# Performance work log

Measured on AMD Instinct MI355X. Metric: run time of the kernel, lower is better.

The kernel has to match this reference:

```python
import jax, jax.numpy as jnp
import numpy as np

D_MODEL = 1024
N_LAYERS = 4
EXPAND = 2
D_CONV = 4
D_STATE = 16
INTER = EXPAND * D_MODEL          # 2048
DT_RANK = (D_MODEL + 15) // 16    # 64, HF: math.ceil(d_model/16)
B_SZ = 4
SEQ = 1024
EPS = 1e-5


def setup_inputs() -> dict:
    key = jax.random.key(0)
    ks = jax.random.split(key, 8)
    nrm = lambda k, s: (0.02 * jax.random.normal(k, s)).astype(jnp.float32)
    return {
        "x": jax.random.normal(ks[0], (B_SZ, SEQ, D_MODEL), dtype=jnp.float32),
        "in_w": nrm(ks[1], (N_LAYERS, 2 * INTER, D_MODEL)),           # in_proj (no bias)
        "conv_w": nrm(ks[2], (N_LAYERS, INTER, D_CONV)),              # depthwise conv weight
        "conv_b": jnp.zeros((N_LAYERS, INTER), jnp.float32),           # conv bias
        "x_w": nrm(ks[3], (N_LAYERS, DT_RANK + 2 * D_STATE, INTER)),  # x_proj (no bias)
        "dt_w": nrm(ks[4], (N_LAYERS, INTER, DT_RANK)),               # dt_proj weight
        "dt_b": jax.random.uniform(ks[5], (N_LAYERS, INTER), minval=-4.0, maxval=-2.0).astype(jnp.float32),
        "A_log": jnp.tile(jnp.log(jnp.arange(1, D_STATE + 1, dtype=jnp.float32)), (N_LAYERS, INTER, 1)),
        "D": jnp.ones((N_LAYERS, INTER), jnp.float32),
        "out_w": nrm(ks[6], (N_LAYERS, D_MODEL, INTER)),              # out_proj (no bias)
        "norm_w": jnp.ones((N_LAYERS, D_MODEL), jnp.float32),          # per-block RMSNorm
        "norm_f_w": jnp.ones((D_MODEL,), jnp.float32),                 # final RMSNorm
    }


def _rmsnorm(x, w):
    return x * jax.lax.rsqrt(jnp.mean(x * x, axis=-1, keepdims=True) + EPS) * w


def _mixer(x, in_w, conv_w, conv_b, x_w, dt_w, dt_b, A_log, Dp, out_w):
    # x: [B, L, d_model]
    Bb = x.shape[0]
    proj = x @ in_w.T                              # [B, L, 2I]
    hs, gate = jnp.split(proj, 2, axis=-1)          # each [B, L, I]
    # causal depthwise conv over time
    hc = hs.transpose(0, 2, 1)                      # [B, I, L]
    hc = jnp.pad(hc, ((0, 0), (0, 0), (D_CONV - 1, 0)))
    hc = jax.lax.conv_general_dilated(
        hc, conv_w[:, None, :], (1,), 'VALID',
        dimension_numbers=('NCH', 'OIH', 'NCH'), feature_group_count=INTER)
    hc = hc + conv_b[None, :, None]
    u = jax.nn.silu(hc).transpose(0, 2, 1)          # [B, L, I]
    ssm = u @ x_w.T                                 # [B, L, dt_rank + 2N]
    dt, Bm, Cm = jnp.split(ssm, [DT_RANK, DT_RANK + D_STATE], axis=-1)
    dt = jax.nn.softplus(dt @ dt_w.T + dt_b)        # [B, L, I]
    A = -jnp.exp(A_log)                             # [I, N]

    def step(state, xs):
        dt_t, B_t, C_t, u_t = xs                    # [B,I], [B,N], [B,N], [B,I]
        dA = jnp.exp(dt_t[:, :, None] * A[None])    # [B, I, N]
        state = dA * state + (dt_t * u_t)[:, :, None] * B_t[:, None, :]
        y = jnp.einsum('bin,bn->bi', state, C_t)
        return state, y

    init = jnp.zeros((Bb, INTER, D_STATE), x.dtype)
    xs = (dt.transpose(1, 0, 2), Bm.transpose(1, 0, 2),
          Cm.transpose(1, 0, 2), u.transpose(1, 0, 2))
    _, ys = jax.lax.scan(step, init, xs)            # ys: [L, B, I]
    y = ys.transpose(1, 0, 2) + u * Dp              # skip term D * u
    y = y * jax.nn.silu(gate)
    return y @ out_w.T                              # [B, L, d_model]


def reference(x, in_w, conv_w, conv_b, x_w, dt_w, dt_b, A_log, D, out_w, norm_w, norm_f_w):
    h = x
    for l in range(N_LAYERS):
        h = h + _mixer(_rmsnorm(h, norm_w[l]), in_w[l], conv_w[l], conv_b[l],
                       x_w[l], dt_w[l], dt_b[l], A_log[l], D[l], out_w[l])
    return _rmsnorm(h, norm_f_w)
```

## Files before the change

### kernel.cpp

```cpp
#include <hip/hip_runtime.h>
#include <hip/hip_bf16.h>
#include <math.h>

#define D_MODEL 1024
#define N_LAYERS 4
#define INTER 2048
#define D_CONV 4
#define D_STATE 16
#define DT_RANK 64
#define B_SZ 4
#define SEQ 1024
#define TOK (B_SZ*SEQ)
#define XROWS 128
#define EPSV 1e-5f
#define GCH 64
#define TC (SEQ/GCH)
#define KSPL 8
#define OSPL 2

typedef unsigned short u16;
typedef unsigned int u32;
typedef __attribute__((ext_vector_type(8))) short bf16x8;
typedef __attribute__((ext_vector_type(4))) short s16x4;
typedef __attribute__((ext_vector_type(4))) float f32x4;

__device__ __forceinline__ u16 f2b(float f) {
    union { float f; unsigned u; } v; v.f = f;
    unsigned r = v.u + 0x7fffu + ((v.u >> 16) & 1u);
    return (u16)(r >> 16);
}
__device__ __forceinline__ float b2f(u16 h) {
    union { unsigned u; float f; } v; v.u = ((unsigned)h) << 16;
    return v.f;
}
__device__ __forceinline__ float silu(float x) {
    return x / (1.f + __expf(-x));
}
__device__ __forceinline__ void gload16(const void* g, void* l) {
    __builtin_amdgcn_global_load_lds(
        (const __attribute__((address_space(1))) void*)g,
        (__attribute__((address_space(3))) void*)l, 16, 0, 0);
}

__global__ __launch_bounds__(512, 2)
void gemm256_k(const u16* __restrict__ A, const u16* __restrict__ B,
               u16* __restrict__ C, int K, int ldc)
{
    __shared__ u16 lds[2][2][256 * 64];
    const int tid  = threadIdx.x;
    const int lane = tid & 63;
    const int wid  = tid >> 6;
    const int wr   = wid >> 2;
    const int wc   = wid & 3;
    const int row0 = blockIdx.y * 256;
    const int col0 = blockIdx.x * 256;
    const int r16   = lane & 15;
    const int khalf = lane >> 4;

    auto stage = [&](int buf, int k0) {
#pragma unroll
        for (int l = 0; l < 8; ++l) {
            int op = l >> 2;
            int c  = tid + (l & 3) * 512;
            int r  = c >> 3;
            int ds = c & 7;
            int sc = (ds ^ (r & 7)) * 8;
            const u16* src = op ? &B[(size_t)(col0 + r) * K + k0 + sc]
                                : &A[(size_t)(row0 + r) * K + k0 + sc];
            gload16(src, &lds[buf][op][c * 8]);
        }
    };
    auto rdA = [&](int buf, int mrow, int ks) -> bf16x8 {
        int row  = wr * 128 + mrow + r16;
        int phys = ((ks << 2) | khalf) ^ (row & 7);
        return *(const bf16x8*)&lds[buf][0][row * 64 + phys * 8];
    };
    auto rdB = [&](int buf, int nrow, int ks) -> bf16x8 {
        int row  = wc * 64 + nrow + r16;
        int phys = ((ks << 2) | khalf) ^ (row & 7);
        return *(const bf16x8*)&lds[buf][1][row * 64 + phys * 8];
    };

    f32x4 acc[8][4];
#pragma unroll
    for (int m = 0; m < 8; ++m)
#pragma unroll
        for (int n = 0; n < 4; ++n)
            acc[m][n] = (f32x4)0.f;

    bf16x8 af[4][2], bf2[2][2];

#define PHASE_MFMA(MH, NH, VMDRAIN) do {                                      \
    asm volatile("s_waitcnt lgkmcnt(0)" ::: "memory");                        \
    __builtin_amdgcn_sched_barrier(0);                                        \
    __builtin_amdgcn_s_setprio(1);                                            \
    _Pragma("unroll")                                                         \
    for (int ks = 0; ks < 2; ++ks)                                            \
        _Pragma("unroll")                                                     \
        for (int m = 0; m < 4; ++m)                                           \
            _Pragma("unroll")                                                 \
            for (int n = 0; n < 2; ++n)                                       \
                acc[(MH)*4+m][(NH)*2+n] =                                     \
                    __builtin_amdgcn_mfma_f32_16x16x32_bf16(                  \
                        af[m][ks], bf2[n][ks], acc[(MH)*4+m][(NH)*2+n],0,0,0);\
    __builtin_amdgcn_s_setprio(0);                                            \
    if (VMDRAIN) { asm volatile("s_waitcnt vmcnt(0)" ::: "memory"); }         \
    __builtin_amdgcn_s_barrier();                                             \
} while (0)

    const int nt = K >> 6;
    stage(0, 0);
    asm volatile("s_waitcnt vmcnt(0)" ::: "memory");
    __builtin_amdgcn_s_barrier();

    for (int j = 0; j < nt; ++j) {
        const int buf = j & 1;
        if (j + 1 < nt) stage(buf ^ 1, (j + 1) << 6);
#pragma unroll
        for (int m = 0; m < 4; ++m) {
            af[m][0] = rdA(buf, m * 16, 0); af[m][1] = rdA(buf, m * 16, 1);
        }
#pragma unroll
        for (int n = 0; n < 2; ++n) {
            bf2[n][0] = rdB(buf, n * 16, 0); bf2[n][1] = rdB(buf, n * 16, 1);
        }
        __builtin_amdgcn_s_barrier();
        PHASE_MFMA(0, 0, 0);
#pragma unroll
        for (int n = 0; n < 2; ++n) {
            bf2[n][0] = rdB(buf, 32 + n * 16, 0); bf2[n][1] = rdB(buf, 32 + n * 16, 1);
        }
        __builtin_amdgcn_s_barrier();
        PHASE_MFMA(0, 1, 0);
#pragma unroll
        for (int m = 0; m < 4; ++m) {
            af[m][0] = rdA(buf, 64 + m * 16, 0); af[m][1] = rdA(buf, 64 + m * 16, 1);
        }
        __builtin_amdgcn_s_barrier();
        PHASE_MFMA(1, 1, 0);
#pragma unroll
        for (int n = 0; n < 2; ++n) {
            bf2[n][0] = rdB(buf, n * 16, 0); bf2[n][1] = rdB(buf, n * 16, 1);
        }
        __builtin_amdgcn_s_barrier();
        PHASE_MFMA(1, 0, 1);
    }
#undef PHASE_MFMA

    const int orow = row0 + wr * 128;
    const int ocol = col0 + wc * 64;
#pragma unroll
    for (int am = 0; am < 8; ++am)
#pragma unroll
        for (int an = 0; an < 4; ++an)
#pragma unroll
            for (int r = 0; r < 4; ++r) {
                int rr = orow + am * 16 + khalf * 4 + r;
                int cc = ocol + an * 16 + r16;
                C[(size_t)rr * ldc + cc] = f2b(acc[am][an][r]);
            }
}

template<int EPI, int NPX = 1>
__global__ __launch_bounds__(256)
void gemm_bt(const u16* __restrict__ A, const u16* __restrict__ B,
             void* __restrict__ C, const float* __restrict__ aux,
             int K, int lda, int ldc, size_t pstride)
{
    __shared__ u16 As[3][128 * 32];
    __shared__ u16 Bs[3][128 * 32];
    const int tid  = threadIdx.x;
    const int lane = tid & 63;
    const int w    = tid >> 6;
    const int wr   = w >> 1, wc = w & 1;
    const int row0 = blockIdx.y * 128;
    int col0 = blockIdx.x * 128;
    if (EPI == 4) {
        int part = blockIdx.x / NPX;
        col0 = (blockIdx.x % NPX) * 128;
        A += (size_t)part * K;
        B += (size_t)part * K;
        C = (void*)((float*)C + (size_t)part * pstride);
    }
    const int r16   = lane & 15;
    const int khalf = lane >> 4;
    const int kslot = khalf ^ ((r16 >> 1) & 3);

    auto stage = [&](int buf, int k0) {
#pragma unroll
        for (int c = 0; c < 2; ++c) {
            int chunk = tid + c * 256;
            int r  = chunk >> 2;
            int j  = chunk & 3;
            int k8 = (j ^ ((r >> 1) & 3)) * 8;
            gload16(&A[(size_t)(row0 + r) * lda + k0 + k8], &As[buf][chunk * 8]);
            gload16(&B[(size_t)(col0 + r) * lda + k0 + k8], &Bs[buf][chunk * 8]);
        }
    };

    f32x4 acc[4][4];
#pragma unroll
    for (int m = 0; m < 4; ++m)
#pragma unroll
        for (int n = 0; n < 4; ++n)
            acc[m][n] = (f32x4)0.f;

    const int nt = K >> 5;
    stage(0, 0);
    if (nt > 1) stage(1, 32);

    int cur = 0, sb = 2;
    for (int t = 0; t < nt; ++t) {
        if (t + 2 < nt) {
            stage(sb, (t + 2) << 5);
            asm volatile("s_waitcnt vmcnt(8)" ::: "memory");
        } else if (t + 1 < nt) {
            asm volatile("s_waitcnt vmcnt(4)" ::: "memory");
        } else {
            asm volatile("s_waitcnt vmcnt(0)" ::: "memory");
        }
        __builtin_amdgcn_s_barrier();

        bf16x8 af[4], bfr[4];
#pragma unroll
        for (int m = 0; m < 4; ++m)
            af[m]  = *(const bf16x8*)&As[cur][(wr * 64 + m * 16 + r16) * 32 + kslot * 8];
#pragma unroll
        for (int n = 0; n < 4; ++n)
            bfr[n] = *(const bf16x8*)&Bs[cur][(wc * 64 + n * 16 + r16) * 32 + kslot * 8];
#pragma unroll
        for (int m = 0; m < 4; ++m)
#pragma unroll
            for (int n = 0; n < 4; ++n)
                acc[m][n] = __builtin_amdgcn_mfma_f32_16x16x32_bf16(
                    af[m], bfr[n], acc[m][n], 0, 0, 0);

        __builtin_amdgcn_sched_barrier(0);
        asm volatile("s_waitcnt lgkmcnt(0)" ::: "memory");
        __builtin_amdgcn_s_barrier();
        cur = (cur == 2) ? 0 : cur + 1;
        sb  = (sb  == 2) ? 0 : sb  + 1;
    }

    const int orow = row0 + wr * 64;
    const int ocol = col0 + wc * 64;
#pragma unroll
    for (int m = 0; m < 4; ++m)
#pragma unroll
        for (int n = 0; n < 4; ++n) {
#pragma unroll
            for (int r = 0; r < 4; ++r) {
                int rr = orow + m * 16 + khalf * 4 + r;
                int cc = ocol + n * 16 + r16;
                float v = acc[m][n][r];
                size_t o = (size_t)rr * ldc + cc;
                if (EPI == 0 || EPI == 4) {
                    ((float*)C)[o] = v;
                } else if (EPI == 2) {
                    float x = v + aux[cc];
                    float sp = (x > 20.f) ? x : log1pf(__expf(x));
                    ((u16*)C)[o] = f2b(sp);
                }
            }
        }
}

__global__ __launch_bounds__(256)
void xred_k(const float* __restrict__ part, float* __restrict__ ssm,
            u16* __restrict__ dtr)
{
    int idx = blockIdx.x * 256 + threadIdx.x;
    int row = idx >> 5;
    int col = (idx & 31) * 4;
    size_t o = (size_t)row * XROWS + col;
    const size_t stride = (size_t)TOK * XROWS;
    f32x4 v = *(const f32x4*)&part[o];
#pragma unroll
    for (int p = 1; p < KSPL; ++p)
        v += *(const f32x4*)&part[o + p * stride];
    *(f32x4*)&ssm[o] = v;
    if (col < DT_RANK) {
        s16x4 d;
#pragma unroll
        for (int j = 0; j < 4; ++j) d[j] = (short)f2b(v[j]);
        *(s16x4*)&dtr[(size_t)row * DT_RANK + col] = d;
    }
}

template<int OUTBF>
__global__ __launch_bounds__(256)
void rmsnorm_k(const float* __restrict__ in, const float* __restrict__ w,
               void* __restrict__ out)
{
    __shared__ float red[4];
    const int row = blockIdx.x;
    const int tid = threadIdx.x;
    const float* r = in + (size_t)row * D_MODEL;
    f32x4 v = *(const f32x4*)&r[tid * 4];
    float ss = v[0]*v[0] + v[1]*v[1] + v[2]*v[2] + v[3]*v[3];
#pragma unroll
    for (int m = 32; m >= 1; m >>= 1) ss += __shfl_xor(ss, m, 64);
    if ((tid & 63) == 0) red[tid >> 6] = ss;
    __syncthreads();
    if (tid == 0) {
        float s = red[0] + red[1] + red[2] + red[3];
        red[0] = rsqrtf(s / (float)D_MODEL + EPSV);
    }
    __syncthreads();
    float sc = red[0];
    if (OUTBF) {
        u16* o = (u16*)out + (size_t)row * D_MODEL + tid * 4;
#pragma unroll
        for (int j = 0; j < 4; ++j) o[j] = f2b(v[j] * sc * w[tid * 4 + j]);
    } else {
        float* o = (float*)out + (size_t)row * D_MODEL + tid * 4;
#pragma unroll
        for (int j = 0; j < 4; ++j) o[j] = v[j] * sc * w[tid * 4 + j];
    }
}

template<int OUTBF, int WRITEH>
__global__ __launch_bounds__(256)
void rmsnorm_res_k(const float* __restrict__ hin, const float* __restrict__ p,
                   const float* __restrict__ w, float* __restrict__ hout,
                   void* __restrict__ out)
{
    __shared__ float red[4];
    const int row = blockIdx.x;
    const int tid = threadIdx.x;
    const size_t o4 = (size_t)row * D_MODEL + tid * 4;
    f32x4 v  = *(const f32x4*)&hin[o4];
    f32x4 p0 = *(const f32x4*)&p[o4];
    f32x4 p1 = *(const f32x4*)&p[(size_t)TOK * D_MODEL + o4];
    v += p0 + p1;
    if (WRITEH) *(f32x4*)&hout[o4] = v;
    float ss = v[0]*v[0] + v[1]*v[1] + v[2]*v[2] + v[3]*v[3];
#pragma unroll
    for (int m = 32; m >= 1; m >>= 1) ss += __shfl_xor(ss, m, 64);
    if ((tid & 63) == 0) red[tid >> 6] = ss;
    __syncthreads();
    if (tid == 0) {
        float s = red[0] + red[1] + red[2] + red[3];
        red[0] = rsqrtf(s / (float)D_MODEL + EPSV);
    }
    __syncthreads();
    float sc = red[0];
    if (OUTBF) {
        u16* o = (u16*)out + o4;
#pragma unroll
        for (int j = 0; j < 4; ++j) o[j] = f2b(v[j] * sc * w[tid * 4 + j]);
    } else {
        float* o = (float*)out + o4;
#pragma unroll
        for (int j = 0; j < 4; ++j) o[j] = v[j] * sc * w[tid * 4 + j];
    }
}

__global__ __launch_bounds__(256)
void conv_silu_k(const u16* __restrict__ projbf, const float* __restrict__ w,
                 const float* __restrict__ bias, u16* __restrict__ ubf)
{
    const int row = blockIdx.x;
    const int t   = row & (SEQ - 1);
    const int i0  = threadIdx.x * 8;
    float acc[8];
    {
        f32x4 b0 = *(const f32x4*)&bias[i0];
        f32x4 b1 = *(const f32x4*)&bias[i0 + 4];
#pragma unroll
        for (int j = 0; j < 4; ++j) { acc[j] = b0[j]; acc[j + 4] = b1[j]; }
    }
    f32x4 wv[8];
#pragma unroll
    for (int j = 0; j < 8; ++j)
        wv[j] = *(const f32x4*)&w[(i0 + j) * 4];
#pragma unroll
    for (int k = 0; k < 4; ++k) {
        int tt = t - 3 + k;
        if (tt >= 0) {
            bf16x8 hv = *(const bf16x8*)&projbf[(size_t)(row - 3 + k) * 4096 + i0];
#pragma unroll
            for (int j = 0; j < 8; ++j)
                acc[j] += b2f((u16)hv[j]) * wv[j][k];
        }
    }
    bf16x8 o;
#pragma unroll
    for (int j = 0; j < 8; ++j)
        o[j] = (short)f2b(silu(acc[j]));
    *(bf16x8*)&ubf[(size_t)row * INTER + i0] = o;
}

__global__ __launch_bounds__(256)
void achk_k(const float* __restrict__ Alog, int* __restrict__ flags)
{
    int idx = blockIdx.x * 256 + threadIdx.x;
    if (idx >= N_LAYERS * INTER * D_STATE) return;
    int l = idx / (INTER * D_STATE);
    int n = idx & (D_STATE - 1);
    float ref = logf((float)(n + 1));
    if (fabsf(Alog[idx] - ref) > 1e-4f) atomicAnd(&flags[l], 0);
}

#define POWCH(W, p) \
    float p##2=(W)*(W), p##3=p##2*(W), p##4=p##2*p##2, p##5=p##4*(W),        \
          p##6=p##4*p##2, p##7=p##4*p##3, p##8=p##4*p##4, p##9=p##8*(W),     \
          p##10=p##8*p##2, p##11=p##8*p##3, p##12=p##8*p##4, p##13=p##8*p##5,\
          p##14=p##8*p##6, p##15=p##8*p##7, p##16=p##8*p##8;

#define SUPD(S, B, du, w1) \
    S[0]=w1*S[0]+du*B[0][0];   S[1]=w1##2*S[1]+du*B[0][1];                   \
    S[2]=w1##3*S[2]+du*B[0][2];  S[3]=w1##4*S[3]+du*B[0][3];                 \
    S[4]=w1##5*S[4]+du*B[1][0];  S[5]=w1##6*S[5]+du*B[1][1];                 \
    S[6]=w1##7*S[6]+du*B[1][2];  S[7]=w1##8*S[7]+du*B[1][3];                 \
    S[8]=w1##9*S[8]+du*B[2][0];  S[9]=w1##10*S[9]+du*B[2][1];                \
    S[10]=w1##11*S[10]+du*B[2][2]; S[11]=w1##12*S[11]+du*B[2][3];            \
    S[12]=w1##13*S[12]+du*B[3][0]; S[13]=w1##14*S[13]+du*B[3][1];            \
    S[14]=w1##15*S[14]+du*B[3][2]; S[15]=w1##16*S[15]+du*B[3][3];

#define YDOT(S, Cv) \
    (S[0]*Cv[0][0]+S[1]*Cv[0][1]+S[2]*Cv[0][2]+S[3]*Cv[0][3]                 \
    +S[4]*Cv[1][0]+S[5]*Cv[1][1]+S[6]*Cv[1][2]+S[7]*Cv[1][3]                 \
    +S[8]*Cv[2][0]+S[9]*Cv[2][1]+S[10]*Cv[2][2]+S[11]*Cv[2][3]               \
    +S[12]*Cv[3][0]+S[13]*Cv[3][1]+S[14]*Cv[3][2]+S[15]*Cv[3][3])

__global__ __launch_bounds__(256)
void scan1_k(const u16* __restrict__ dtbf, const u16* __restrict__ ubf,
             const float* __restrict__ ssm, const float* __restrict__ Alog,
             const int* __restrict__ flag,
             float* __restrict__ cst, float* __restrict__ dts)
{
    __shared__ float Bsh[TC][D_STATE];
    const int tid = threadIdx.x;
    const int i2  = blockIdx.x * 256 + tid;
    const int c0  = i2 * 2;
    const int g   = blockIdx.y;
    const int b   = blockIdx.z;
    const int t0  = g * TC;
    {
        int t = tid >> 4, n = tid & 15;
        Bsh[t][n] = ssm[(size_t)(b * SEQ + t0 + t) * XROWS + DT_RANK + n];
    }
    __syncthreads();

    float s0[D_STATE], s1[D_STATE];
#pragma unroll
    for (int n = 0; n < D_STATE; ++n) { s0[n] = 0.f; s1[n] = 0.f; }
    float ds0 = 0.f, ds1 = 0.f;

    const u32* dtp = (const u32*)dtbf + ((size_t)(b * SEQ + t0) * INTER >> 1) + i2;
    const u32* up  = (const u32*)ubf  + ((size_t)(b * SEQ + t0) * INTER >> 1) + i2;

    if (flag[0]) {
#pragma unroll
        for (int t = 0; t < TC; ++t) {
            u32 dp = dtp[(size_t)t * (INTER / 2)];
            u32 uq = up[(size_t)t * (INTER / 2)];
            float dta = b2f((u16)dp), dtb = b2f((u16)(dp >> 16));
            float ua  = b2f((u16)uq), ub  = b2f((u16)(uq >> 16));
            float dua = dta * ua, dub = dtb * ub;
            ds0 += dta; ds1 += dtb;
            float wa = __expf(-dta), wb = __expf(-dtb);
            POWCH(wa, wa) POWCH(wb, wb)
            f32x4 Bq[4];
#pragma unroll
            for (int q = 0; q < 4; ++q) Bq[q] = *(const f32x4*)&Bsh[t][q * 4];
            SUPD(s0, Bq, dua, wa)
            SUPD(s1, Bq, dub, wb)
        }
    } else {
        float a0[D_STATE], a1[D_STATE];
#pragma unroll
        for (int n = 0; n < D_STATE; ++n) {
            a0[n] = -__expf(Alog[(size_t)c0 * D_STATE + n]);
            a1[n] = -__expf(Alog[(size_t)(c0 + 1) * D_STATE + n]);
        }
        for (int t = 0; t < TC; ++t) {
            u32 dp = dtp[(size_t)t * (INTER / 2)];
            u32 uq = up[(size_t)t * (INTER / 2)];
            float dta = b2f((u16)dp), dtb = b2f((u16)(dp >> 16));
            float ua  = b2f((u16)uq), ub  = b2f((u16)(uq >> 16));
            float dua = dta * ua, dub = dtb * ub;
            ds0 += dta; ds1 += dtb;
#pragma unroll
            for (int n = 0; n < D_STATE; ++n) {
                float Bn = Bsh[t][n];
                s0[n] = __expf(dta * a0[n]) * s0[n] + dua * Bn;
                s1[n] = __expf(dtb * a1[n]) * s1[n] + dub * Bn;
            }
        }
    }
    size_t o = ((size_t)(b * GCH + g) * INTER + c0) * D_STATE;
#pragma unroll
    for (int n = 0; n < D_STATE; n += 4) {
        f32x4 v0 = { s0[n], s0[n+1], s0[n+2], s0[n+3] };
        f32x4 v1 = { s1[n], s1[n+1], s1[n+2], s1[n+3] };
        *(f32x4*)&cst[o + n] = v0;
        *(f32x4*)&cst[o + D_STATE + n] = v1;
    }
    size_t od = (size_t)(b * GCH + g) * INTER + c0;
    dts[od] = ds0; dts[od + 1] = ds1;
}

__global__ __launch_bounds__(256)
void scan2_k(float* __restrict__ cst, const float* __restrict__ dts,
             const float* __restrict__ Alog)
{
    int idx = blockIdx.x * 256 + threadIdx.x;
    int sub = idx & 3;
    int i   = (idx >> 2) & (INTER - 1);
    int b   = idx >> 13;
    int n0  = sub * 4;
    float a[4];
#pragma unroll
    for (int n = 0; n < 4; ++n)
        a[n] = -__expf(Alog[(size_t)i * D_STATE + n0 + n]);
    f32x4 s = (f32x4)0.f;
    for (int g = 0; g < GCH; ++g) {
        size_t o = ((size_t)(b * GCH + g) * INTER + i) * D_STATE + n0;
        f32x4 tmp = *(const f32x4*)&cst[o];
        *(f32x4*)&cst[o] = s;
        float d = dts[(size_t)(b * GCH + g) * INTER + i];
#pragma unroll
        for (int n = 0; n < 4; ++n)
            s[n] = __expf(a[n] * d) * s[n] + tmp[n];
    }
}

__global__ __launch_bounds__(256)
void scan3_k(const u16* __restrict__ dtbf, const u16* __restrict__ ubf,
             const float* __restrict__ ssm, const u16* __restrict__ projbf,
             const float* __restrict__ Alog, const float* __restrict__ Dp,
             const int* __restrict__ flag,
             const float* __restrict__ sst, u16* __restrict__ ybf)
{
    __shared__ float Bsh[TC][D_STATE];
    __shared__ float Csh[TC][D_STATE];
    const int tid = threadIdx.x;
    const int i2  = blockIdx.x * 256 + tid;
    const int c0  = i2 * 2;
    const int g   = blockIdx.y;
    const int b   = blockIdx.z;
    const int t0  = g * TC;
    {
        int t = tid >> 4, n = tid & 15;
        size_t row = (size_t)(b * SEQ + t0 + t) * XROWS;
        Bsh[t][n] = ssm[row + DT_RANK + n];
        Csh[t][n] = ssm[row + DT_RANK + D_STATE + n];
    }
    __syncthreads();

    const float Da = Dp[c0], Db = Dp[c0 + 1];
    float s0[D_STATE], s1[D_STATE];
    size_t so = ((size_t)(b * GCH + g) * INTER + c0) * D_STATE;
#pragma unroll
    for (int n = 0; n < D_STATE; n += 4) {
        f32x4 v0 = *(const f32x4*)&sst[so + n];
        f32x4 v1 = *(const f32x4*)&sst[so + D_STATE + n];
        s0[n] = v0[0]; s0[n+1] = v0[1]; s0[n+2] = v0[2]; s0[n+3] = v0[3];
        s1[n] = v1[0]; s1[n+1] = v1[1]; s1[n+2] = v1[2]; s1[n+3] = v1[3];
    }

    const u32* dtp = (const u32*)dtbf + ((size_t)(b * SEQ + t0) * INTER >> 1) + i2;
    const u32* up  = (const u32*)ubf  + ((size_t)(b * SEQ + t0) * INTER >> 1) + i2;
    const u32* gp  = (const u32*)projbf + (((size_t)(b * SEQ + t0) * 4096 + INTER) >> 1) + i2;
    u32*       yp  = (u32*)ybf + ((size_t)(b * SEQ + t0) * INTER >> 1) + i2;

    if (flag[0]) {
#pragma unroll
        for (int t = 0; t < TC; ++t) {
            u32 dp = dtp[(size_t)t * (INTER / 2)];
            u32 uq = up[(size_t)t * (INTER / 2)];
            u32 gq = gp[(size_t)t * (4096 / 2)];
            float dta = b2f((u16)dp), dtb = b2f((u16)(dp >> 16));
            float ua  = b2f((u16)uq), ub  = b2f((u16)(uq >> 16));
            float ga  = b2f((u16)gq), gb  = b2f((u16)(gq >> 16));
            float dua = dta * ua, dub = dtb * ub;
            float wa = __expf(-dta), wb = __expf(-dtb);
            POWCH(wa, wa) POWCH(wb, wb)
            f32x4 Bq[4], Cq[4];
#pragma unroll
            for (int q = 0; q < 4; ++q) {
                Bq[q] = *(const f32x4*)&Bsh[t][q * 4];
                Cq[q] = *(const f32x4*)&Csh[t][q * 4];
            }
            SUPD(s0, Bq, dua, wa)
            SUPD(s1, Bq, dub, wb)
            float y0 = YDOT(s0, Cq);
            float y1 = YDOT(s1, Cq);
            y0 = (y0 + Da * ua) * silu(ga);
            y1 = (y1 + Db * ub) * silu(gb);
            yp[(size_t)t * (INTER / 2)] = (u32)f2b(y0) | ((u32)f2b(y1) << 16);
        }
    } else {
        float a0[D_STATE], a1[D_STATE];
#pragma unroll
        for (int n = 0; n < D_STATE; ++n) {
            a0[n] = -__expf(Alog[(size_t)c0 * D_STATE + n]);
            a1[n] = -__expf(Alog[(size_t)(c0 + 1) * D_STATE + n]);
        }
        for (int t = 0; t < TC; ++t) {
            u32 dp = dtp[(size_t)t * (INTER / 2)];
            u32 uq = up[(size_t)t * (INTER / 2)];
            u32 gq = gp[(size_t)t * (4096 / 2)];
            float dta = b2f((u16)dp), dtb = b2f((u16)(dp >> 16));
            float ua  = b2f((u16)uq), ub  = b2f((u16)(uq >> 16));
            float ga  = b2f((u16)gq), gb  = b2f((u16)(gq >> 16));
            float dua = dta * ua, dub = dtb * ub;
            float y0 = 0.f, y1 = 0.f;
#pragma unroll
            for (int n = 0; n < D_STATE; ++n) {
                float Bn = Bsh[t][n], Cn = Csh[t][n];
                s0[n] = __expf(dta * a0[n]) * s0[n] + dua * Bn;
                s1[n] = __expf(dtb * a1[n]) * s1[n] + dub * Bn;
                y0 += s0[n] * Cn; y1 += s1[n] * Cn;
            }
            y0 = (y0 + Da * ua) * silu(ga);
            y1 = (y1 + Db * ub) * silu(gb);
            yp[(size_t)t * (INTER / 2)] = (u32)f2b(y0) | ((u32)f2b(y1) << 16);
        }
    }
}

__global__ __launch_bounds__(256)
void cvt_f2b_k(const float* __restrict__ in, u16* __restrict__ out, int n)
{
    int idx = (blockIdx.x * 256 + threadIdx.x) * 4;
    if (idx >= n) return;
    f32x4 v = *(const f32x4*)&in[idx];
    s16x4 d;
#pragma unroll
    for (int j = 0; j < 4; ++j) d[j] = (short)f2b(v[j]);
    *(s16x4*)&out[idx] = d;
}

__global__ __launch_bounds__(256)
void pad_xw_k(const float* __restrict__ xw, u16* __restrict__ out)
{
    int idx = (blockIdx.x * 256 + threadIdx.x) * 4;
    if (idx >= N_LAYERS * XROWS * INTER) return;
    int l = idx / (XROWS * INTER);
    int r = (idx >> 11) & (XROWS - 1);
    int c = idx & (INTER - 1);
    s16x4 d;
    if (r < 96) {
        f32x4 v = *(const f32x4*)&xw[((size_t)l * 96 + r) * INTER + c];
#pragma unroll
        for (int j = 0; j < 4; ++j) d[j] = (short)f2b(v[j]);
    } else {
        d = (s16x4)0;
    }
    *(s16x4*)&out[idx] = d;
}

extern "C" void kernel_launch(void* const* d_in, const int* in_sizes, int n_in,
                              void* d_out, int out_size, void* d_ws, size_t ws_size,
                              hipStream_t stream)
{
    const float* x      = (const float*)d_in[0];
    const float* in_w   = (const float*)d_in[1];
    const float* conv_w = (const float*)d_in[2];
    const float* conv_b = (const float*)d_in[3];
    const float* x_w    = (const float*)d_in[4];
    const float* dt_w   = (const float*)d_in[5];
    const float* dt_b   = (const float*)d_in[6];
    const float* A_log  = (const float*)d_in[7];
    const float* Dp     = (const float*)d_in[8];
    const float* out_w  = (const float*)d_in[9];
    const float* norm_w = (const float*)d_in[10];
    const float* norm_f = (const float*)d_in[11];

    char* ws = (char*)d_ws;
    size_t off = 0;
    auto alloc = [&](size_t bytes) { char* p = ws + off; off += (bytes + 255) & ~(size_t)255; return p; };

    u16*   inw_bf  = (u16*)  alloc((size_t)N_LAYERS * 4096 * 1024 * 2);
    u16*   xw_bf   = (u16*)  alloc((size_t)N_LAYERS * XROWS * INTER * 2);
    u16*   dtw_bf  = (u16*)  alloc((size_t)N_LAYERS * INTER * DT_RANK * 2);
    u16*   outw_bf = (u16*)  alloc((size_t)N_LAYERS * D_MODEL * INTER * 2);
    float* h       = (float*)alloc((size_t)TOK * D_MODEL * 4);
    u16*   xn_bf   = (u16*)  alloc((size_t)TOK * D_MODEL * 2);
    u16*   proj_bf = (u16*)  alloc((size_t)TOK * 4096 * 2);
    u16*   u_bf    = (u16*)  alloc((size_t)TOK * INTER * 2);
    float* ssm     = (float*)alloc((size_t)TOK * XROWS * 4);
    float* parts   = (float*)alloc((size_t)OSPL * TOK * D_MODEL * 4);
    u16*   dtr_bf  = (u16*)  alloc((size_t)TOK * DT_RANK * 2);
    u16*   dt_bf   = (u16*)  alloc((size_t)TOK * INTER * 2);
    u16*   y_bf    = (u16*)  alloc((size_t)TOK * INTER * 2);
    float* cst     = (float*)alloc((size_t)B_SZ * GCH * INTER * D_STATE * 4);
    float* dts     = (float*)alloc((size_t)B_SZ * GCH * INTER * 4);
    int*   aflags  = (int*)  alloc(N_LAYERS * sizeof(int));
    (void)ws_size; (void)n_in; (void)in_sizes; (void)out_size;

    {
        int n = N_LAYERS * 4096 * 1024;
        cvt_f2b_k<<<n / 1024, 256, 0, stream>>>(in_w, inw_bf, n);
        int np = N_LAYERS * XROWS * INTER;
        pad_xw_k<<<np / 1024, 256, 0, stream>>>(x_w, xw_bf);
        int nd = N_LAYERS * INTER * DT_RANK;
        cvt_f2b_k<<<nd / 1024, 256, 0, stream>>>(dt_w, dtw_bf, nd);
        int no = N_LAYERS * D_MODEL * INTER;
        cvt_f2b_k<<<no / 1024, 256, 0, stream>>>(out_w, outw_bf, no);
        hipMemsetAsync(aflags, 0xFF, N_LAYERS * sizeof(int), stream);
        int na = N_LAYERS * INTER * D_STATE;
        achk_k<<<(na + 255) / 256, 256, 0, stream>>>(A_log, aflags);
    }

    for (int l = 0; l < N_LAYERS; ++l) {
        if (l == 0)
            rmsnorm_k<1><<<TOK, 256, 0, stream>>>(x, norm_w, xn_bf);
        else
            rmsnorm_res_k<1, 1><<<TOK, 256, 0, stream>>>(
                (l == 1) ? x : h, parts, norm_w + (size_t)l * D_MODEL, h, xn_bf);
        gemm256_k<<<dim3(16, 16), 512, 0, stream>>>(
            xn_bf, inw_bf + (size_t)l * 4096 * 1024, proj_bf, 1024, 4096);
        conv_silu_k<<<TOK, 256, 0, stream>>>(
            proj_bf, conv_w + (size_t)l * INTER * D_CONV, conv_b + (size_t)l * INTER, u_bf);
        gemm_bt<4, 1><<<dim3(KSPL, 32), 256, 0, stream>>>(
            u_bf, xw_bf + (size_t)l * XROWS * INTER, parts, nullptr,
            INTER / KSPL, INTER, XROWS, (size_t)TOK * XROWS);
        xred_k<<<(TOK * 32) / 256, 256, 0, stream>>>(parts, ssm, dtr_bf);
        gemm_bt<2><<<dim3(16, 32), 256, 0, stream>>>(
            dtr_bf, dtw_bf + (size_t)l * INTER * DT_RANK, dt_bf,
            dt_b + (size_t)l * INTER, DT_RANK, DT_RANK, INTER, 0);
        scan1_k<<<dim3(INTER / 512, GCH, B_SZ), 256, 0, stream>>>(
            dt_bf, u_bf, ssm, A_log + (size_t)l * INTER * D_STATE, aflags + l, cst, dts);
        scan2_k<<<(B_SZ * INTER * 4) / 256, 256, 0, stream>>>(
            cst, dts, A_log + (size_t)l * INTER * D_STATE);
        scan3_k<<<dim3(INTER / 512, GCH, B_SZ), 256, 0, stream>>>(
            dt_bf, u_bf, ssm, proj_bf, A_log + (size_t)l * INTER * D_STATE,
            Dp + (size_t)l * INTER, aflags + l, cst, y_bf);
        gemm_bt<4, 8><<<dim3(OSPL * 8, 32), 256, 0, stream>>>(
            y_bf, outw_bf + (size_t)l * D_MODEL * INTER, parts, nullptr,
            INTER / OSPL, INTER, D_MODEL, (size_t)TOK * D_MODEL);
    }
    rmsnorm_res_k<0, 0><<<TOK, 256, 0, stream>>>(
        h, parts, norm_f, nullptr, d_out);
}
```

Baseline: 908.2 us.

## Interleave GEMM prefetch loads across MFMA phases and remap block tiles

The next K-tile's global-to-LDS loads are now split into four pairs issued between the MFMA phases, with partial vmcnt waits, instead of all at once at loop start followed by a full drain. The block index is also remapped so tiles are assigned in a chiplet-aware, XCD-interleaved order with a fixed 16-column grid. The aim is to spread memory traffic across the compute phases and improve L2 locality between co-resident blocks. The remap hardcodes a 16-tile-wide grid (N=4096) and assumes the grid size matches, which could break other GEMM shapes using this kernel. The vmcnt bookkeeping is delicate.

```diff
diff --git a/kernel.cpp b/kernel.cpp
--- a/kernel.cpp
+++ b/kernel.cpp
@@ -52,23 +52,28 @@
     const int wid  = tid >> 6;
     const int wr   = wid >> 2;
     const int wc   = wid & 3;
-    const int row0 = blockIdx.y * 256;
-    const int col0 = blockIdx.x * 256;
+    const int hwid = blockIdx.y * gridDim.x + blockIdx.x;
+    const int work = (hwid & 7) * 32 + (hwid >> 3);
+    const int row0 = (work >> 4) * 256;
+    const int col0 = (work & 15) * 256;
     const int r16   = lane & 15;
     const int khalf = lane >> 4;
 
-    auto stage = [&](int buf, int k0) {
-#pragma unroll
-        for (int l = 0; l < 8; ++l) {
-            int op = l >> 2;
-            int c  = tid + (l & 3) * 512;
-            int r  = c >> 3;
-            int ds = c & 7;
-            int sc = (ds ^ (r & 7)) * 8;
-            const u16* src = op ? &B[(size_t)(col0 + r) * K + k0 + sc]
-                                : &A[(size_t)(row0 + r) * K + k0 + sc];
-            gload16(src, &lds[buf][op][c * 8]);
-        }
+    auto ld1 = [&](int buf, int k0, int l) {
+        int op = l >> 2;
+        int c  = tid + (l & 3) * 512;
+        int r  = c >> 3;
+        int ds = c & 7;
+        int sc = (ds ^ (r & 7)) * 8;
+        const u16* src = op ? &B[(size_t)(col0 + r) * K + k0 + sc]
+                            : &A[(size_t)(row0 + r) * K + k0 + sc];
+        gload16(src, &lds[buf][op][c * 8]);
+    };
+    auto stage2 = [&](int buf, int k0, int pair) {
+        if (pair == 0)      { ld1(buf, k0, 0); ld1(buf, k0, 2); }
+        else if (pair == 1) { ld1(buf, k0, 4); ld1(buf, k0, 5); }
+        else if (pair == 2) { ld1(buf, k0, 6); ld1(buf, k0, 7); }
+        else                { ld1(buf, k0, 1); ld1(buf, k0, 3); }
     };
     auto rdA = [&](int buf, int mrow, int ks) -> bf16x8 {
         int row  = wr * 128 + mrow + r16;
@@ -90,7 +95,7 @@
 
     bf16x8 af[4][2], bf2[2][2];
 
-#define PHASE_MFMA(MH, NH, VMDRAIN) do {                                      \
+#define PHASE_MFMA(MH, NH) do {                                               \
     asm volatile("s_waitcnt lgkmcnt(0)" ::: "memory");                        \
     __builtin_amdgcn_sched_barrier(0);                                        \
     __builtin_amdgcn_s_setprio(1);                                            \
@@ -104,18 +109,19 @@
                     __builtin_amdgcn_mfma_f32_16x16x32_bf16(                  \
                         af[m][ks], bf2[n][ks], acc[(MH)*4+m][(NH)*2+n],0,0,0);\
     __builtin_amdgcn_s_setprio(0);                                            \
-    if (VMDRAIN) { asm volatile("s_waitcnt vmcnt(0)" ::: "memory"); }         \
-    __builtin_amdgcn_s_barrier();                                             \
 } while (0)
 
     const int nt = K >> 6;
-    stage(0, 0);
-    asm volatile("s_waitcnt vmcnt(0)" ::: "memory");
+    stage2(0, 0, 0); stage2(0, 0, 1); stage2(0, 0, 2); stage2(0, 0, 3);
+    asm volatile("s_waitcnt vmcnt(2)" ::: "memory");
     __builtin_amdgcn_s_barrier();
 
     for (int j = 0; j < nt; ++j) {
         const int buf = j & 1;
-        if (j + 1 < nt) stage(buf ^ 1, (j + 1) << 6);
+        const int nb  = buf ^ 1;
+        const int k1  = (j + 1) << 6;
+        const bool pf = (j + 1 < nt);
+        if (pf) stage2(nb, k1, 0);
 #pragma unroll
         for (int m = 0; m < 4; ++m) {
             af[m][0] = rdA(buf, m * 16, 0); af[m][1] = rdA(buf, m * 16, 1);
@@ -125,25 +131,35 @@
             bf2[n][0] = rdB(buf, n * 16, 0); bf2[n][1] = rdB(buf, n * 16, 1);
         }
         __builtin_amdgcn_s_barrier();
-        PHASE_MFMA(0, 0, 0);
+        PHASE_MFMA(0, 0);
+        __builtin_amdgcn_s_barrier();
+        if (pf) stage2(nb, k1, 1);
 #pragma unroll
         for (int n = 0; n < 2; ++n) {
             bf2[n][0] = rdB(buf, 32 + n * 16, 0); bf2[n][1] = rdB(buf, 32 + n * 16, 1);
         }
         __builtin_amdgcn_s_barrier();
-        PHASE_MFMA(0, 1, 0);
+        PHASE_MFMA(0, 1);
+        if (pf) { asm volatile("s_waitcnt vmcnt(4)" ::: "memory"); }
+        else    { asm volatile("s_waitcnt vmcnt(0)" ::: "memory"); }
+        __builtin_amdgcn_s_barrier();
+        if (pf) stage2(nb, k1, 2);
 #pragma unroll
         for (int m = 0; m < 4; ++m) {
             af[m][0] = rdA(buf, 64 + m * 16, 0); af[m][1] = rdA(buf, 64 + m * 16, 1);
         }
         __builtin_amdgcn_s_barrier();
-        PHASE_MFMA(1, 1, 0);
+        PHASE_MFMA(1, 1);
+        __builtin_amdgcn_s_barrier();
+        if (pf) stage2(nb, k1, 3);
 #pragma unroll
         for (int n = 0; n < 2; ++n) {
             bf2[n][0] = rdB(buf, n * 16, 0); bf2[n][1] = rdB(buf, n * 16, 1);
         }
         __builtin_amdgcn_s_barrier();
-        PHASE_MFMA(1, 0, 1);
+        PHASE_MFMA(1, 0);
+        asm volatile("s_waitcnt vmcnt(2)" ::: "memory");
+        __builtin_amdgcn_s_barrier();
     }
 #undef PHASE_MFMA
 
```

New measurement: 900.7 us. No clear change (-0.8%).
